# Kernel optimization log

Hardware: AMD Instinct MI355X
Metric: run time of the kernel (lower is better)

Reference implementation:

```python
import jax, jax.numpy as jnp
import numpy as np

H = 1024        # hidden_units
NH = 16         # num_heads
HD = H // NH    # head_dim = 64
B = 32
S = 500
MAX_SEQ = 500
ROPE_BASE = 10000.0


def setup_inputs() -> dict:
    key = jax.random.key(0)
    ks = jax.random.split(key, 16)
    s = 1.0 / np.sqrt(H)
    inp = {
        "query": jax.random.normal(ks[0], (B, S, H), jnp.float32),
        "key":   jax.random.normal(ks[1], (B, S, H), jnp.float32),
        "value": jax.random.normal(ks[2], (B, S, H), jnp.float32),
        "attn_mask": jax.random.randint(ks[3], (B, S), 0, 2).astype(bool),
        "Wq": jax.random.uniform(ks[4], (H, H), jnp.float32, -s, s),
        "bq": jax.random.uniform(ks[5], (H,), jnp.float32, -s, s),
        "Wk": jax.random.uniform(ks[6], (H, H), jnp.float32, -s, s),
        "bk": jax.random.uniform(ks[7], (H,), jnp.float32, -s, s),
        "Wv": jax.random.uniform(ks[8], (H, H), jnp.float32, -s, s),
        "bv": jax.random.uniform(ks[9], (H,), jnp.float32, -s, s),
        "Wo": jax.random.uniform(ks[10], (H, H), jnp.float32, -s, s),
        "bo": jax.random.uniform(ks[11], (H,), jnp.float32, -s, s),
        # rel_pos_bias embedding table: [2*max_seq_len-1, num_heads]
        "rel_emb": jax.random.normal(ks[12], (2 * MAX_SEQ - 1, NH), jnp.float32),
    }
    return inp


def _rope_tables(seq_len, head_dim, dtype):
    inv_freq = 1.0 / (ROPE_BASE ** (jnp.arange(0, head_dim, 2, dtype=jnp.float32) / head_dim))
    t = jnp.arange(seq_len, dtype=jnp.float32)
    freqs = t[:, None] * inv_freq[None, :]           # [S, HD/2]
    emb = jnp.concatenate([freqs, freqs], axis=-1)   # [S, HD]
    return jnp.cos(emb).astype(dtype), jnp.sin(emb).astype(dtype)


def _apply_rope(x, cos, sin):
    # x: [B, NH, S, HD]; even/odd slicing variant from source
    x_rot = jnp.concatenate([-x[..., 1::2], x[..., 0::2]], axis=-1)
    return x * cos + x_rot * sin


def reference(query, key, value, attn_mask, Wq, bq, Wk, bk, Wv, bv, Wo, bo, rel_emb):
    b, s, _ = query.shape
    Q = (query @ Wq.T + bq).reshape(b, s, NH, HD).transpose(0, 2, 1, 3)  # [B,NH,S,HD]
    K = (key   @ Wk.T + bk).reshape(b, s, NH, HD).transpose(0, 2, 1, 3)
    V = (value @ Wv.T + bv).reshape(b, s, NH, HD).transpose(0, 2, 1, 3)

    cos, sin = _rope_tables(s, HD, Q.dtype)  # [S,HD]
    Q = _apply_rope(Q, cos, sin)
    K = _apply_rope(K, cos, sin)

    # relative-position bias: [1, NH, S, S]
    pos = jnp.arange(s)[:, None] - jnp.arange(s)[None, :]
    rel_idx = jnp.clip(pos + MAX_SEQ - 1, 0, 2 * MAX_SEQ - 2)
    rel_bias = rel_emb[rel_idx].transpose(2, 0, 1)[None]  # [1,NH,S,S]

    # key-padding mask -> additive float mask [B,1,1,S]
    mask_bias = jnp.where(attn_mask[:, None, None, :], 0.0, -jnp.inf).astype(Q.dtype)

    scale = 1.0 / np.sqrt(HD)
    scores = jnp.einsum('bhqd,bhkd->bhqk', Q, K) * scale + mask_bias + rel_bias
    attn = jax.nn.softmax(scores, axis=-1)
    out = jnp.einsum('bhqk,bhkd->bhqd', attn, V)
    out = out.transpose(0, 2, 1, 3).reshape(b, s, H)
    out = jnp.clip(out, -30.0, 30.0)
    return out @ Wo.T + bo
```

## Files before the change

### kernel.cpp

```cpp
#include <hip/hip_runtime.h>
#include <math.h>


typedef unsigned short u16;
typedef unsigned int   u32;
typedef unsigned char  u8;
using bf16x8 = __attribute__((ext_vector_type(8))) short;
using f32x4  = __attribute__((ext_vector_type(4))) float;
using f32x2  = __attribute__((ext_vector_type(2))) float;
using u16x4  = __attribute__((ext_vector_type(4))) unsigned short;

#define DEV __device__ __forceinline__

#if __has_builtin(__builtin_amdgcn_exp2f)
#define EXP2(x) __builtin_amdgcn_exp2f(x)
#else
#define EXP2(x) exp2f(x)
#endif

DEV u16 f2bf(float f) {
  union { float f; u32 u; } c; c.f = f;
  u32 u = c.u;
  return (u16)((u + 0x7FFFu + ((u >> 16) & 1u)) >> 16);
}
DEV float bf2f(u16 h) {
  union { u32 u; float f; } c; c.u = ((u32)h) << 16;
  return c.f;
}
DEV u32 cvtpk(float a, float b) {
  u32 r;
  asm("v_cvt_pk_bf16_f32 %0, %1, %2" : "=v"(r) : "v"(a), "v"(b));
  return r;
}

DEV void async16(void* l, const void* g) {
  __builtin_amdgcn_global_load_lds(
      (__attribute__((address_space(1))) unsigned int*)g,
      (__attribute__((address_space(3))) unsigned int*)l, 16, 0, 0);
}

__global__ __launch_bounds__(512) void build_gather(const void* __restrict__ mraw,
                                                    u16* __restrict__ karr,
                                                    int* __restrict__ kept) {
  const int b = blockIdx.x;
  const int t = threadIdx.x;
  const int lane = t & 63, wave = t >> 6;
  __shared__ int s_li, s_lf;
  __shared__ int wbase[8];
  __shared__ int wpop[8];
  if (t == 0) { s_li = 0; s_lf = 0; }
  __syncthreads();
  const u32* w = (const u32*)mraw;
  int li = 0, lf = 0;
  for (int g = t; g < 4000; g += 512) {
    u32 v = w[g];
    li |= !(v == 0u || v == 1u);
    lf |= !(v == 0u || v == 0x3F800000u);
  }
  if (li) atomicOr(&s_li, 1);
  if (lf) atomicOr(&s_lf, 1);
  __syncthreads();
  const int mode = (!s_li) ? 0 : ((!s_lf) ? 1 : 2);
  int v = 0;
  if (t < 500) {
    if (mode == 0)      v = ((const int*)mraw)[b * 500 + t] != 0;
    else if (mode == 1) v = (((const float*)mraw)[b * 500 + t] != 0.0f);
    else                v = ((const u8*)mraw)[b * 500 + t] != 0;
  }
  unsigned long long bal = __ballot(v != 0);
  karr[b * 512 + t] = 0xFFFF;
  if (lane == 0) wpop[wave] = __popcll(bal);
  __syncthreads();
  if (t == 0) {
    int s = 0;
    for (int ww = 0; ww < 8; ++ww) { wbase[ww] = s; s += wpop[ww]; }
    kept[b] = s;
  }
  __syncthreads();
  if (v) {
    int rank = wbase[wave] + __popcll(bal & ((1ull << lane) - 1ull));
    karr[b * 512 + rank] = (u16)t;
  }
}

__global__ __launch_bounds__(256) void rope_table(float* __restrict__ tab) {
  int idx = blockIdx.x * 256 + threadIdx.x;
  if (idx >= 16000) return;
  int s = idx >> 5, j = idx & 31;
  float ang = (float)s * exp2f(-(float)j * 0.41524100f);
  float sn, cs;
  sincosf(ang, &sn, &cs);
  tab[idx * 2] = cs;
  tab[idx * 2 + 1] = sn;
}

__global__ __launch_bounds__(256) void cvt_w4(const float* __restrict__ w0,
                                              const float* __restrict__ w1,
                                              const float* __restrict__ w2,
                                              const float* __restrict__ w3,
                                              u16* __restrict__ dst) {
  const float* src = (blockIdx.y == 0) ? w0 : (blockIdx.y == 1) ? w1
                    : (blockIdx.y == 2) ? w2 : w3;
  int i = blockIdx.x * 256 + threadIdx.x;
  f32x4 f = *(const f32x4*)(src + (size_t)i * 4);
  u16x4 o;
  o[0] = f2bf(f[0]); o[1] = f2bf(f[1]); o[2] = f2bf(f[2]); o[3] = f2bf(f[3]);
  *(u16x4*)(dst + (size_t)blockIdx.y * 1048576 + (size_t)i * 4) = o;
}

__global__ __launch_bounds__(256) void cvt_f32_bf16(const float* __restrict__ src,
                                                    u16* __restrict__ dst, int n4) {
  int i = blockIdx.x * 256 + threadIdx.x;
  int stride = gridDim.x * 256;
  for (; i < n4; i += stride) {
    f32x4 f = *(const f32x4*)(src + (size_t)i * 4);
    u16x4 o;
    o[0] = f2bf(f[0]); o[1] = f2bf(f[1]); o[2] = f2bf(f[2]); o[3] = f2bf(f[3]);
    *(u16x4*)(dst + (size_t)i * 4) = o;
  }
}

__global__ __launch_bounds__(256) void gathercvt2(const float* __restrict__ srcK,
                                                  const float* __restrict__ srcV,
                                                  const u16* __restrict__ karr,
                                                  const int* __restrict__ kept,
                                                  u16* __restrict__ dstK,
                                                  u16* __restrict__ dstV) {
  const int b = blockIdx.y;
  const int r = blockIdx.x * 2 + (threadIdx.x >> 7);
  if (r >= kept[b]) return;
  const float* src = blockIdx.z ? srcV : srcK;
  u16* dst = blockIdx.z ? dstV : dstK;
  const int c = (threadIdx.x & 127) * 8;
  const int tok = karr[b * 512 + r];
  const float* s = src + ((size_t)b * 500 + tok) * 1024 + c;
  f32x4 f0 = *(const f32x4*)s;
  f32x4 f1 = *(const f32x4*)(s + 4);
  u16 o[8];
  o[0] = f2bf(f0[0]); o[1] = f2bf(f0[1]); o[2] = f2bf(f0[2]); o[3] = f2bf(f0[3]);
  o[4] = f2bf(f1[0]); o[5] = f2bf(f1[1]); o[6] = f2bf(f1[2]); o[7] = f2bf(f1[3]);
  *(bf16x8*)(dst + ((size_t)b * 512 + r) * 1024 + c) = *(bf16x8*)o;
}

DEV void gemm_core(const u16* __restrict__ A, size_t abase,
                   const u16* __restrict__ W,
                   int m0, int n0, int Mloc,
                   u16* AS, u16* BS, f32x4 (&acc)[4][4], int tid) {
  const int wave = tid >> 6;
  const int wr = wave >> 1, wc = wave & 1;
  const int fr = tid & 15, fo = (tid >> 4) & 3;
  const int fr2 = fr >> 1;
  const int aslot = ((4 * (fr & 1) + fo) ^ fr2) * 8;
  const int ATILE = 128 * 64;
  const int BTILE = 64 * 64;

#pragma unroll
  for (int mi = 0; mi < 4; ++mi)
#pragma unroll
    for (int ni = 0; ni < 4; ++ni)
#pragma unroll
      for (int j = 0; j < 4; ++j) acc[mi][ni][j] = 0.f;

  auto STG = [&](int t, int buf) {
    u16* sA = &AS[buf * ATILE];
    u16* sB = &BS[buf * BTILE];
#pragma unroll
    for (int i = 0; i < 2; ++i) {
      int c = i * 512 + tid;
      int r = c >> 3, v = (c & 7) ^ (r & 7);
      int ar = min(m0 + 2 * r + (v >> 2), Mloc - 1);
      async16(&sA[c * 8], A + abase + (size_t)ar * 1024 + t * 32 + (v & 3) * 8);
    }
    {
      int c = tid;
      int r = c >> 3, v = (c & 7) ^ (r & 7);
      int nr = n0 + 2 * r + (v >> 2);
      async16(&sB[c * 8], W + (size_t)nr * 1024 + t * 32 + (v & 3) * 8);
    }
  };

  STG(0, 0);
  asm volatile("s_waitcnt vmcnt(0)" ::: "memory");
  __builtin_amdgcn_sched_barrier(0);
  __builtin_amdgcn_s_barrier();

  int cur = 0;
  for (int t = 0; t < 32; ++t) {
    if (t + 1 < 32) STG(t + 1, cur ^ 1);
    const u16* a0 = &AS[cur * ATILE];
    const u16* b0 = &BS[cur * BTILE];
    bf16x8 a[4], b[4];
#pragma unroll
    for (int mi = 0; mi < 4; ++mi)
      a[mi] = *(const bf16x8*)&a0[(wr * 32 + mi * 8 + fr2) * 64 + aslot];
#pragma unroll
    for (int ni = 0; ni < 4; ++ni)
      b[ni] = *(const bf16x8*)&b0[(wc * 32 + ni * 8 + fr2) * 64 + aslot];
    asm volatile("s_waitcnt lgkmcnt(0)" ::: "memory");
    __builtin_amdgcn_sched_barrier(0);
    __builtin_amdgcn_s_setprio(1);
#pragma unroll
    for (int mi = 0; mi < 4; ++mi)
#pragma unroll
      for (int ni = 0; ni < 4; ++ni)
        acc[mi][ni] = __builtin_amdgcn_mfma_f32_16x16x32_bf16(a[mi], b[ni], acc[mi][ni], 0, 0, 0);
    __builtin_amdgcn_s_setprio(0);
    asm volatile("s_waitcnt vmcnt(0)" ::: "memory");
    __builtin_amdgcn_sched_barrier(0);
    __builtin_amdgcn_s_barrier();
    cur ^= 1;
  }
  __syncthreads();
}

__global__ __launch_bounds__(512, 4) void gemm_fused(
    const u16* __restrict__ Xq, const u16* __restrict__ XkC, const u16* __restrict__ XvC,
    const u16* __restrict__ Wb,
    const float* __restrict__ bq, const float* __restrict__ bk, const float* __restrict__ bv,
    u16* __restrict__ Qro, u16* __restrict__ PkC, u16* __restrict__ PvC,
    const float* __restrict__ tabg, const int* __restrict__ keptp) {
  __shared__ __attribute__((aligned(16))) u16 AS[2 * 128 * 64];
  __shared__ __attribute__((aligned(16))) u16 BS[2 * 64 * 64];
  const int bid = blockIdx.x;
  const int tid = threadIdx.x;
  const int wave = tid >> 6;
  const int wr = wave >> 1, wc = wave & 1;
  const int fr = tid & 15, fo = (tid >> 4) & 3;

  f32x4 acc[4][4];

  if (bid < 504) {
    const int swz = (bid & 7) * 63 + (bid >> 3);
    const int m0 = (swz >> 3) * 256;
    const int n0 = (swz & 7) * 128;
    gemm_core(Xq, 0, Wb, m0, n0, 16000, AS, BS, acc, tid);

    float* fw = (float*)&AS[0] + wave * 1024;
    const int hh = (n0 >> 6) + wc;
    const int lane = tid & 63;
    const int row = lane >> 2;
    const int jb = (lane & 3) * 8;
    float bvv[4];
#pragma unroll
    for (int ni = 0; ni < 4; ++ni) bvv[ni] = bq[n0 + wc * 64 + ni * 16 + fr];
#pragma unroll
    for (int mi = 0; mi < 4; ++mi) {
#pragma unroll
      for (int ni = 0; ni < 4; ++ni)
#pragma unroll
        for (int r = 0; r < 4; ++r)
          fw[(fo * 4 + r) * 64 + ni * 16 + fr] = acc[mi][ni][r] + bvv[ni];
      int m = m0 + wr * 64 + mi * 16 + row;
      if (m < 16000) {
        int bb = (u32)m / 500u;
        int ss = m - bb * 500;
        u16* dst = Qro + (((size_t)(bb * 16 + hh)) * 500 + ss) * 64;
        bf16x8 va, vb;
#pragma unroll
        for (int p = 0; p < 8; ++p) {
          int j = jb + p;
          float x0 = fw[row * 64 + j];
          float x1 = fw[row * 64 + 32 + j];
          float xe = fw[row * 64 + 2 * j];
          float xo = fw[row * 64 + 2 * j + 1];
          f32x2 cn = *(const f32x2*)(tabg + (ss * 32 + j) * 2);
          va[p] = (short)f2bf(x0 * cn[0] - xo * cn[1]);
          vb[p] = (short)f2bf(x1 * cn[0] + xe * cn[1]);
        }
        *(bf16x8*)(dst + jb) = va;
        *(bf16x8*)(dst + 32 + jb) = vb;
      }
      __builtin_amdgcn_s_barrier();
    }
  } else {
    const bool isV = (bid >= 1016);
    const int local = isV ? (bid - 1016) : (bid - 504);
    const u16* A = isV ? XvC : XkC;
    const u16* W = Wb + (isV ? 2 : 1) * 1048576;
    const float* bias = isV ? bv : bk;
    u16* Cout = isV ? PvC : PkC;
    const int swz = (local & 7) * 64 + (local >> 3);
    const int mb = swz >> 3;
    const int n0 = (swz & 7) * 128;
    const int b = mb >> 1, rb = mb & 1;
    const int kb = keptp[b];
    if (rb * 256 >= kb) return;
    const int m0 = rb * 256;
    gemm_core(A, (size_t)b * 512 * 1024, W, m0, n0, kb, AS, BS, acc, tid);

    u16* bw = (u16*)&AS[0] + wave * 2048;
#pragma unroll
    for (int mi = 0; mi < 4; ++mi) {
#pragma unroll
      for (int ni = 0; ni < 4; ++ni) {
        float bvs = bias[n0 + wc * 64 + ni * 16 + fr];
#pragma unroll
        for (int r = 0; r < 4; ++r)
          bw[(fo * 4 + r) * 64 + ni * 16 + fr] = f2bf(acc[mi][ni][r] + bvs);
      }
      int lane = tid & 63;
      int ro = lane >> 2, ch = lane & 3;
      int m = m0 + wr * 64 + mi * 16 + ro;
      bf16x8 v0 = *(const bf16x8*)&bw[ro * 64 + ch * 16];
      bf16x8 v1 = *(const bf16x8*)&bw[ro * 64 + ch * 16 + 8];
      if (m < kb) {
        u16* dst = Cout + ((size_t)b * 512 + m) * 1024 + n0 + wc * 64 + ch * 16;
        *(bf16x8*)dst = v0;
        *(bf16x8*)(dst + 8) = v1;
      }
    }
  }
}

__global__ __launch_bounds__(512, 4) void gemm_out(const u16* __restrict__ A,
                                                   const u16* __restrict__ W,
                                                   const float* __restrict__ bias,
                                                   float* __restrict__ Cout) {
  __shared__ __attribute__((aligned(16))) u16 AS[2 * 128 * 64];
  __shared__ __attribute__((aligned(16))) u16 BS[2 * 64 * 64];
  const int bid = blockIdx.x;
  const int tid = threadIdx.x;
  const int wave = tid >> 6;
  const int wr = wave >> 1, wc = wave & 1;
  const int fr = tid & 15, fo = (tid >> 4) & 3;
  const int swz = (bid & 7) * 63 + (bid >> 3);
  const int m0 = (swz >> 3) * 256;
  const int n0 = (swz & 7) * 128;

  f32x4 acc[4][4];
  gemm_core(A, 0, W, m0, n0, 16000, AS, BS, acc, tid);

  float* fw = (float*)&AS[0] + wave * 1024;
#pragma unroll
  for (int mi = 0; mi < 4; ++mi) {
#pragma unroll
    for (int ni = 0; ni < 4; ++ni) {
      float bv = bias[n0 + wc * 64 + ni * 16 + fr];
#pragma unroll
      for (int r = 0; r < 4; ++r)
        fw[(fo * 4 + r) * 64 + ni * 16 + fr] = acc[mi][ni][r] + bv;
    }
    int lane = tid & 63;
    int ro = lane >> 2, ch = lane & 3;
    int m = m0 + wr * 64 + mi * 16 + ro;
    f32x4 v0 = *(const f32x4*)&fw[ro * 64 + ch * 16];
    f32x4 v1 = *(const f32x4*)&fw[ro * 64 + ch * 16 + 4];
    f32x4 v2 = *(const f32x4*)&fw[ro * 64 + ch * 16 + 8];
    f32x4 v3 = *(const f32x4*)&fw[ro * 64 + ch * 16 + 12];
    if (m < 16000) {
      float* dst = Cout + (size_t)m * 1024 + n0 + wc * 64 + ch * 16;
      *(f32x4*)dst = v0;
      *(f32x4*)(dst + 4) = v1;
      *(f32x4*)(dst + 8) = v2;
      *(f32x4*)(dst + 12) = v3;
    }
  }
}

__global__ __launch_bounds__(256) void gather_k(const u16* __restrict__ PkC,
                                                const float* __restrict__ tab,
                                                const u16* __restrict__ karr,
                                                const int* __restrict__ kept,
                                                u16* __restrict__ Ktg) {
  const int tile = blockIdx.x;
  const int bh = blockIdx.y;
  const int h = bh & 15, b = bh >> 4;
  if (tile * 64 >= kept[b]) return;
  char* out = (char*)(Ktg + ((size_t)bh * 8 + tile) * 4096);
  const int tid = threadIdx.x;
#pragma unroll
  for (int i = 0; i < 8; ++i) {
    int item = i * 256 + tid;
    int row = item >> 5, j = item & 31;
    int rk = tile * 64 + row;
    int tok = karr[b * 512 + rk];
    int sw = (row & 7) << 4;
    u16 o0 = 0, o1 = 0;
    if (tok != 0xFFFF) {
      const u16* src = PkC + ((size_t)b * 512 + rk) * 1024 + h * 64;
      float x0 = bf2f(src[j]);
      float x1 = bf2f(src[32 + j]);
      float xe = bf2f(src[2 * j]);
      float xo = bf2f(src[2 * j + 1]);
      f32x2 cn = *(const f32x2*)(tab + (tok * 32 + j) * 2);
      o0 = f2bf(x0 * cn[0] - xo * cn[1]);
      o1 = f2bf(x1 * cn[0] + xe * cn[1]);
    }
    *(u16*)(out + row * 128 + ((2 * j) ^ sw)) = o0;
    *(u16*)(out + row * 128 + ((64 + 2 * j) ^ sw)) = o1;
  }
}

__global__ __launch_bounds__(256) void gather_v(const u16* __restrict__ PvC,
                                                const u16* __restrict__ karr,
                                                const int* __restrict__ kept,
                                                u16* __restrict__ Vtg) {
  const int tile = blockIdx.x;
  const int bh = blockIdx.y;
  const int h = bh & 15, b = bh >> 4;
  if (tile * 64 >= kept[b]) return;
  const int tid = threadIdx.x;
  __shared__ __attribute__((aligned(16))) u16 Vl[64 * 64];
#pragma unroll
  for (int i = 0; i < 2; ++i) {
    int chunk = i * 256 + tid;
    int slot = chunk >> 3, seg = chunk & 7;
    int rk = tile * 64 + slot;
    int tok = karr[b * 512 + rk];
    bf16x8 v;
#pragma unroll
    for (int p = 0; p < 8; ++p) v[p] = 0;
    if (tok != 0xFFFF)
      v = *(const bf16x8*)(PvC + ((size_t)b * 512 + rk) * 1024 + h * 64 + seg * 8);
    *(bf16x8*)&Vl[slot * 64 + seg * 8] = v;
  }
  __syncthreads();
  u16* out = Vtg + ((size_t)bh * 8 + tile) * 4096;
#pragma unroll
  for (int i = 0; i < 2; ++i) {
    int chunk = i * 256 + tid;
    int d = chunk >> 3, c16 = chunk & 7;
    int k0 = ((c16 * 16) ^ ((d & 7) << 4)) >> 1;
    bf16x8 v;
#pragma unroll
    for (int p = 0; p < 8; ++p) v[p] = (short)Vl[(k0 + p) * 64 + d];
    *(bf16x8*)(out + chunk * 8) = v;
  }
}

__global__ __launch_bounds__(512) void attn_kernel(const u16* __restrict__ Qr,
                                                   const u16* __restrict__ Ktg,
                                                   const u16* __restrict__ Vtg,
                                                   const float* __restrict__ rel_emb,
                                                   const u16* __restrict__ karr,
                                                   const int* __restrict__ kept,
                                                   u16* __restrict__ AO) {
  const int bid = blockIdx.x;
  const int bh = ((bid >> 5) << 3) | (bid & 7);
  const int qb = (bid >> 3) & 3;
  const int h = bh & 15, b = bh >> 4;
  const int q0 = qb * 128;
  const int tid = threadIdx.x;
  const int wave = tid >> 6;
  const int fr = tid & 15, fo = (tid >> 4) & 3;

  __shared__ __attribute__((aligned(16))) u16 Ks[2][4096];
  __shared__ __attribute__((aligned(16))) u16 Vs[2][4096];
  __shared__ __attribute__((aligned(16))) u16 Pl[8][1024];
  __shared__ float rel2[640];
  __shared__ u16 okk[512];

  const int nt = (kept[b] + 63) >> 6;
  const float LOG2E = 1.44269504f;
  for (int i = tid; i < 640; i += 512) {
    int g = min(max(q0 - 12 + i, 0), 998);
    rel2[i] = (i == 0) ? -1e30f : rel_emb[g * 16 + h] * LOG2E;
  }
  okk[tid] = karr[b * 512 + tid];

  const int qloc = wave * 16 + fr;
  const int qc = qloc + 511;
  const u16* Qb = Qr + ((size_t)bh * 500 + min(q0 + qloc, 499)) * 64;
  bf16x8 qf0 = *(const bf16x8*)(Qb + fo * 8);
  bf16x8 qf1 = *(const bf16x8*)(Qb + 32 + fo * 8);

  f32x4 o[4];
#pragma unroll
  for (int nf = 0; nf < 4; ++nf)
#pragma unroll
    for (int j = 0; j < 4; ++j) o[nf][j] = 0.f;
  float mrun = -1e30f, lrun = 0.f;

  const u16* Kb = Ktg + (size_t)bh * 32768;
  const u16* Vb = Vtg + (size_t)bh * 32768;
  const int sw = (fr & 7) << 4;
  const float SC = 0.18033688f;

  if (nt > 0) {
    async16(&Ks[0][tid * 8], Kb + tid * 8);
    async16(&Vs[0][tid * 8], Vb + tid * 8);
  }
  __syncthreads();

  for (int t = 0; t < nt; ++t) {
    const int cur = t & 1;
    if (t + 1 < nt) {
      async16(&Ks[cur ^ 1][tid * 8], Kb + (t + 1) * 4096 + tid * 8);
      async16(&Vs[cur ^ 1][tid * 8], Vb + (t + 1) * 4096 + tid * 8);
    }
    const char* Kt = (const char*)(cur ? &Ks[1][0] : &Ks[0][0]);
    const char* Vt = (const char*)(cur ? &Vs[1][0] : &Vs[0][0]);

    f32x4 sacc[4];
    __builtin_amdgcn_s_setprio(1);
#pragma unroll
    for (int nf = 0; nf < 4; ++nf) {
#pragma unroll
      for (int jj = 0; jj < 4; ++jj) sacc[nf][jj] = 0.f;
      int rb = (nf * 16 + fr) * 128;
      bf16x8 kb0 = *(const bf16x8*)(Kt + rb + ((fo * 16) ^ sw));
      bf16x8 kb1 = *(const bf16x8*)(Kt + rb + ((64 + fo * 16) ^ sw));
      sacc[nf] = __builtin_amdgcn_mfma_f32_16x16x32_bf16(kb0, qf0, sacc[nf], 0, 0, 0);
      sacc[nf] = __builtin_amdgcn_mfma_f32_16x16x32_bf16(kb1, qf1, sacc[nf], 0, 0, 0);
    }
    __builtin_amdgcn_s_setprio(0);

    float p2[4][4];
    float pmax = -3e30f;
#pragma unroll
    for (int nf = 0; nf < 4; ++nf) {
      u16x4 ok4 = *(const u16x4*)&okk[t * 64 + nf * 16 + fo * 4];
#pragma unroll
      for (int r = 0; r < 4; ++r) {
        int idx2 = max(qc - (int)ok4[r], 0);
        float s2 = fmaf(sacc[nf][r], SC, rel2[idx2]);
        p2[nf][r] = s2;
        pmax = fmaxf(pmax, s2);
      }
    }
    pmax = fmaxf(pmax, __shfl_xor(pmax, 16, 64));
    pmax = fmaxf(pmax, __shfl_xor(pmax, 32, 64));

    if (!__all(pmax <= mrun + 8.0f)) {
      float mnew = fmaxf(mrun, pmax);
      float scl = EXP2(mrun - mnew);
      lrun *= scl;
#pragma unroll
      for (int nf = 0; nf < 4; ++nf)
#pragma unroll
        for (int r = 0; r < 4; ++r) o[nf][r] *= scl;
      mrun = mnew;
    }

    float lsum = 0.f;
#pragma unroll
    for (int nf = 0; nf < 4; ++nf) {
      float e0 = EXP2(p2[nf][0] - mrun);
      float e1 = EXP2(p2[nf][1] - mrun);
      float e2 = EXP2(p2[nf][2] - mrun);
      float e3 = EXP2(p2[nf][3] - mrun);
      lsum += (e0 + e1) + (e2 + e3);
      uint2 w; w.x = cvtpk(e0, e1); w.y = cvtpk(e2, e3);
      *(uint2*)((char*)&Pl[wave][0] + fr * 128 + ((nf * 32 + fo * 8) ^ sw)) = w;
    }
    lsum += __shfl_xor(lsum, 16, 64);
    lsum += __shfl_xor(lsum, 32, 64);
    lrun += lsum;

    bf16x8 pa0 = *(const bf16x8*)((char*)&Pl[wave][0] + fr * 128 + ((fo * 16) ^ sw));
    bf16x8 pa1 = *(const bf16x8*)((char*)&Pl[wave][0] + fr * 128 + ((64 + fo * 16) ^ sw));
    __builtin_amdgcn_s_setprio(1);
#pragma unroll
    for (int nf = 0; nf < 4; ++nf) {
      int rb = (nf * 16 + fr) * 128;
      bf16x8 vb0 = *(const bf16x8*)(Vt + rb + ((fo * 16) ^ sw));
      bf16x8 vb1 = *(const bf16x8*)(Vt + rb + ((64 + fo * 16) ^ sw));
      o[nf] = __builtin_amdgcn_mfma_f32_16x16x32_bf16(vb0, pa0, o[nf], 0, 0, 0);
      o[nf] = __builtin_amdgcn_mfma_f32_16x16x32_bf16(vb1, pa1, o[nf], 0, 0, 0);
    }
    __builtin_amdgcn_s_setprio(0);
    __syncthreads();
  }

  float inv = (lrun > 0.f) ? 1.f / lrun : 0.f;
#pragma unroll
  for (int nf = 0; nf < 4; ++nf) {
    float v0 = fminf(fmaxf(o[nf][0] * inv, -30.f), 30.f);
    float v1 = fminf(fmaxf(o[nf][1] * inv, -30.f), 30.f);
    float v2 = fminf(fmaxf(o[nf][2] * inv, -30.f), 30.f);
    float v3 = fminf(fmaxf(o[nf][3] * inv, -30.f), 30.f);
    uint2 w; w.x = cvtpk(v0, v1); w.y = cvtpk(v2, v3);
    *(uint2*)((char*)&Pl[wave][0] + fr * 128 + ((nf * 32 + fo * 8) ^ sw)) = w;
  }
  {
    int lane = tid & 63;
    int ro = lane >> 2, c = lane & 3;
    int swr = (ro & 7) << 4;
    const char* Pw = (const char*)&Pl[wave][0];
    bf16x8 v0 = *(const bf16x8*)(Pw + ro * 128 + ((c * 32) ^ swr));
    bf16x8 v1 = *(const bf16x8*)(Pw + ro * 128 + ((c * 32 + 16) ^ swr));
    int token = q0 + wave * 16 + ro;
    if (token < 500) {
      u16* dst = AO + (size_t)(b * 500 + token) * 1024 + h * 64 + c * 16;
      *(bf16x8*)dst = v0;
      *(bf16x8*)(dst + 8) = v1;
    }
  }
}

extern "C" void kernel_launch(void* const* d_in, const int* in_sizes, int n_in,
                              void* d_out, int out_size, void* d_ws, size_t ws_size,
                              hipStream_t stream) {
  const float* query = (const float*)d_in[0];
  const float* key_  = (const float*)d_in[1];
  const float* value = (const float*)d_in[2];
  const void*  mask  = d_in[3];
  const float* Wq = (const float*)d_in[4];
  const float* bq = (const float*)d_in[5];
  const float* Wk = (const float*)d_in[6];
  const float* bk = (const float*)d_in[7];
  const float* Wv = (const float*)d_in[8];
  const float* bv = (const float*)d_in[9];
  const float* Wo = (const float*)d_in[10];
  const float* bo = (const float*)d_in[11];
  const float* rel = (const float*)d_in[12];

  char* ws = (char*)d_ws;
  const size_t SLOT = 33554432;
  u16* Wb = (u16*)ws;
  char* Aq = ws + 8388608;
  char* Bq = Aq + SLOT;
  char* Cq = Bq + SLOT;
  char* Dq = Cq + SLOT;
  char* Eq = Dq + SLOT;
  char* MISC = Eq + SLOT;
  u16* karr  = (u16*)(MISC + 65536);
  int* kept  = (int*)(MISC + 131072);
  float* tab = (float*)(MISC + 131584);
  u16* Qro = (u16*)d_out;

  build_gather<<<32, 512, 0, stream>>>(mask, karr, kept);
  rope_table<<<63, 256, 0, stream>>>(tab);
  cvt_w4<<<dim3(1024, 4), 256, 0, stream>>>(Wq, Wk, Wv, Wo, Wb);
  cvt_f32_bf16<<<2048, 256, 0, stream>>>(query, (u16*)Aq, 4096000);
  gathercvt2<<<dim3(256, 32, 2), 256, 0, stream>>>(key_, value, karr, kept,
                                                   (u16*)Bq, (u16*)Cq);

  gemm_fused<<<1528, 512, 0, stream>>>((u16*)Aq, (u16*)Bq, (u16*)Cq, Wb,
                                       bq, bk, bv,
                                       Qro, (u16*)Eq, (u16*)Dq, tab, kept);

  gather_k<<<dim3(8, 512), 256, 0, stream>>>((u16*)Eq, tab, karr, kept, (u16*)Cq);
  gather_v<<<dim3(8, 512), 256, 0, stream>>>((u16*)Dq, karr, kept, (u16*)Aq);

  attn_kernel<<<2048, 512, 0, stream>>>(Qro, (u16*)Cq, (u16*)Aq, rel,
                                        karr, kept, (u16*)Bq);

  gemm_out<<<504, 512, 0, stream>>>((u16*)Bq, Wb + 3 * 1048576, bo, (float*)d_out);
}
```

Measured before the change: 280.0 us.

## Fuse K RoPE/tiling and V transpose into the K/V projection GEMM epilogue

The K and V projection epilogues now write straight into the swizzled per-head tile layouts the attention kernel consumes. K gets RoPE applied with the gathered token positions, and V is transposed through padded shared memory. This removes the separate gather_k and gather_v kernels, along with the round trip of the projected K/V through global memory and two launches. In exchange the GEMM epilogue grows, with more scattered stores and extra barriers. It also adds a barrier to the gemm_out epilogue loop and merges the shared arrays into one buffer.

```diff
diff --git a/kernel.cpp b/kernel.cpp
--- a/kernel.cpp
+++ b/kernel.cpp
@@ -217,15 +217,18 @@
     const u16* __restrict__ Xq, const u16* __restrict__ XkC, const u16* __restrict__ XvC,
     const u16* __restrict__ Wb,
     const float* __restrict__ bq, const float* __restrict__ bk, const float* __restrict__ bv,
-    u16* __restrict__ Qro, u16* __restrict__ PkC, u16* __restrict__ PvC,
-    const float* __restrict__ tabg, const int* __restrict__ keptp) {
-  __shared__ __attribute__((aligned(16))) u16 AS[2 * 128 * 64];
-  __shared__ __attribute__((aligned(16))) u16 BS[2 * 64 * 64];
+    u16* __restrict__ Qro, u16* __restrict__ Ktg, u16* __restrict__ Vtg,
+    const float* __restrict__ tabg, const u16* __restrict__ karr,
+    const int* __restrict__ keptp) {
+  __shared__ __attribute__((aligned(16))) u16 SH[2 * 128 * 64 + 2 * 64 * 64];
+  u16* AS = &SH[0];
+  u16* BS = &SH[2 * 128 * 64];
   const int bid = blockIdx.x;
   const int tid = threadIdx.x;
   const int wave = tid >> 6;
   const int wr = wave >> 1, wc = wave & 1;
   const int fr = tid & 15, fo = (tid >> 4) & 3;
+  const int lane = tid & 63;
 
   f32x4 acc[4][4];
 
@@ -235,9 +238,8 @@
     const int n0 = (swz & 7) * 128;
     gemm_core(Xq, 0, Wb, m0, n0, 16000, AS, BS, acc, tid);
 
-    float* fw = (float*)&AS[0] + wave * 1024;
+    float* fw = (float*)&SH[0] + wave * 1024;
     const int hh = (n0 >> 6) + wc;
-    const int lane = tid & 63;
     const int row = lane >> 2;
     const int jb = (lane & 3) * 8;
     float bvv[4];
@@ -278,7 +280,6 @@
     const u16* A = isV ? XvC : XkC;
     const u16* W = Wb + (isV ? 2 : 1) * 1048576;
     const float* bias = isV ? bv : bk;
-    u16* Cout = isV ? PvC : PkC;
     const int swz = (local & 7) * 64 + (local >> 3);
     const int mb = swz >> 3;
     const int n0 = (swz & 7) * 128;
@@ -288,25 +289,75 @@
     const int m0 = rb * 256;
     gemm_core(A, (size_t)b * 512 * 1024, W, m0, n0, kb, AS, BS, acc, tid);
 
-    u16* bw = (u16*)&AS[0] + wave * 2048;
-#pragma unroll
-    for (int mi = 0; mi < 4; ++mi) {
-#pragma unroll
-      for (int ni = 0; ni < 4; ++ni) {
-        float bvs = bias[n0 + wc * 64 + ni * 16 + fr];
-#pragma unroll
-        for (int r = 0; r < 4; ++r)
-          bw[(fo * 4 + r) * 64 + ni * 16 + fr] = f2bf(acc[mi][ni][r] + bvs);
+    float* fw = (float*)&SH[0] + wave * 1056;
+    const int hh = (n0 >> 6) + wc;
+    float bvv[4];
+#pragma unroll
+    for (int ni = 0; ni < 4; ++ni) bvv[ni] = bias[n0 + wc * 64 + ni * 16 + fr];
+
+    if (!isV) {
+      const int row = lane >> 2;
+      const int jb = (lane & 3) * 8;
+#pragma unroll
+      for (int mi = 0; mi < 4; ++mi) {
+#pragma unroll
+        for (int ni = 0; ni < 4; ++ni)
+#pragma unroll
+          for (int r = 0; r < 4; ++r)
+            fw[(fo * 4 + r) * 66 + ni * 16 + fr] = acc[mi][ni][r] + bvv[ni];
+        int rk = m0 + wr * 64 + mi * 16 + row;
+        int tile = rk >> 6, rin = rk & 63;
+        int swk = (rin & 7) << 4;
+        if (tile * 64 < kb) {
+          char* outp = (char*)(Ktg + (((size_t)(b * 16 + hh)) * 8 + tile) * 4096) + rin * 128;
+          bf16x8 va, vb;
+          if (rk < kb) {
+            int tok = karr[b * 512 + rk];
+#pragma unroll
+            for (int p = 0; p < 8; ++p) {
+              int j = jb + p;
+              float x0 = fw[row * 66 + j];
+              float x1 = fw[row * 66 + 32 + j];
+              float xe = fw[row * 66 + 2 * j];
+              float xo = fw[row * 66 + 2 * j + 1];
+              f32x2 cn = *(const f32x2*)(tabg + (tok * 32 + j) * 2);
+              va[p] = (short)f2bf(x0 * cn[0] - xo * cn[1]);
+              vb[p] = (short)f2bf(x1 * cn[0] + xe * cn[1]);
+            }
+          } else {
+#pragma unroll
+            for (int p = 0; p < 8; ++p) { va[p] = 0; vb[p] = 0; }
+          }
+          *(bf16x8*)(outp + ((2 * jb) ^ swk)) = va;
+          *(bf16x8*)(outp + ((64 + 2 * jb) ^ swk)) = vb;
+        }
+        __builtin_amdgcn_s_barrier();
       }
-      int lane = tid & 63;
-      int ro = lane >> 2, ch = lane & 3;
-      int m = m0 + wr * 64 + mi * 16 + ro;
-      bf16x8 v0 = *(const bf16x8*)&bw[ro * 64 + ch * 16];
-      bf16x8 v1 = *(const bf16x8*)&bw[ro * 64 + ch * 16 + 8];
-      if (m < kb) {
-        u16* dst = Cout + ((size_t)b * 512 + m) * 1024 + n0 + wc * 64 + ch * 16;
-        *(bf16x8*)dst = v0;
-        *(bf16x8*)(dst + 8) = v1;
+    } else {
+      const int d = lane;
+      const int swv = (d & 7) << 4;
+#pragma unroll
+      for (int mi = 0; mi < 4; ++mi) {
+#pragma unroll
+        for (int ni = 0; ni < 4; ++ni)
+#pragma unroll
+          for (int r = 0; r < 4; ++r)
+            fw[(fo * 4 + r) * 66 + ni * 16 + fr] = acc[mi][ni][r] + bvv[ni];
+        int rk0 = m0 + wr * 64 + mi * 16;
+        int tile = rk0 >> 6, rin0 = rk0 & 63;
+        if (tile * 64 < kb) {
+          char* rowp = (char*)(Vtg + (((size_t)(b * 16 + hh)) * 8 + tile) * 4096) + d * 128;
+          bf16x8 va, vb;
+#pragma unroll
+          for (int t2 = 0; t2 < 8; ++t2)
+            va[t2] = (rk0 + t2 < kb) ? (short)f2bf(fw[t2 * 66 + d]) : (short)0;
+#pragma unroll
+          for (int t2 = 0; t2 < 8; ++t2)
+            vb[t2] = (rk0 + 8 + t2 < kb) ? (short)f2bf(fw[(8 + t2) * 66 + d]) : (short)0;
+          *(bf16x8*)(rowp + ((2 * rin0) ^ swv)) = va;
+          *(bf16x8*)(rowp + ((2 * rin0 + 16) ^ swv)) = vb;
+        }
+        __builtin_amdgcn_s_barrier();
       }
     }
   }
@@ -316,8 +367,9 @@
                                                    const u16* __restrict__ W,
                                                    const float* __restrict__ bias,
                                                    float* __restrict__ Cout) {
-  __shared__ __attribute__((aligned(16))) u16 AS[2 * 128 * 64];
-  __shared__ __attribute__((aligned(16))) u16 BS[2 * 64 * 64];
+  __shared__ __attribute__((aligned(16))) u16 SH[2 * 128 * 64 + 2 * 64 * 64];
+  u16* AS = &SH[0];
+  u16* BS = &SH[2 * 128 * 64];
   const int bid = blockIdx.x;
   const int tid = threadIdx.x;
   const int wave = tid >> 6;
@@ -330,7 +382,7 @@
   f32x4 acc[4][4];
   gemm_core(A, 0, W, m0, n0, 16000, AS, BS, acc, tid);
 
-  float* fw = (float*)&AS[0] + wave * 1024;
+  float* fw = (float*)&SH[0] + wave * 1024;
 #pragma unroll
   for (int mi = 0; mi < 4; ++mi) {
 #pragma unroll
@@ -354,77 +406,7 @@
       *(f32x4*)(dst + 8) = v2;
       *(f32x4*)(dst + 12) = v3;
     }
-  }
-}
-
-__global__ __launch_bounds__(256) void gather_k(const u16* __restrict__ PkC,
-                                                const float* __restrict__ tab,
-                                                const u16* __restrict__ karr,
-                                                const int* __restrict__ kept,
-                                                u16* __restrict__ Ktg) {
-  const int tile = blockIdx.x;
-  const int bh = blockIdx.y;
-  const int h = bh & 15, b = bh >> 4;
-  if (tile * 64 >= kept[b]) return;
-  char* out = (char*)(Ktg + ((size_t)bh * 8 + tile) * 4096);
-  const int tid = threadIdx.x;
-#pragma unroll
-  for (int i = 0; i < 8; ++i) {
-    int item = i * 256 + tid;
-    int row = item >> 5, j = item & 31;
-    int rk = tile * 64 + row;
-    int tok = karr[b * 512 + rk];
-    int sw = (row & 7) << 4;
-    u16 o0 = 0, o1 = 0;
-    if (tok != 0xFFFF) {
-      const u16* src = PkC + ((size_t)b * 512 + rk) * 1024 + h * 64;
-      float x0 = bf2f(src[j]);
-      float x1 = bf2f(src[32 + j]);
-      float xe = bf2f(src[2 * j]);
-      float xo = bf2f(src[2 * j + 1]);
-      f32x2 cn = *(const f32x2*)(tab + (tok * 32 + j) * 2);
-      o0 = f2bf(x0 * cn[0] - xo * cn[1]);
-      o1 = f2bf(x1 * cn[0] + xe * cn[1]);
-    }
-    *(u16*)(out + row * 128 + ((2 * j) ^ sw)) = o0;
-    *(u16*)(out + row * 128 + ((64 + 2 * j) ^ sw)) = o1;
-  }
-}
-
-__global__ __launch_bounds__(256) void gather_v(const u16* __restrict__ PvC,
-                                                const u16* __restrict__ karr,
-                                                const int* __restrict__ kept,
-                                                u16* __restrict__ Vtg) {
-  const int tile = blockIdx.x;
-  const int bh = blockIdx.y;
-  const int h = bh & 15, b = bh >> 4;
-  if (tile * 64 >= kept[b]) return;
-  const int tid = threadIdx.x;
-  __shared__ __attribute__((aligned(16))) u16 Vl[64 * 64];
-#pragma unroll
-  for (int i = 0; i < 2; ++i) {
-    int chunk = i * 256 + tid;
-    int slot = chunk >> 3, seg = chunk & 7;
-    int rk = tile * 64 + slot;
-    int tok = karr[b * 512 + rk];
-    bf16x8 v;
-#pragma unroll
-    for (int p = 0; p < 8; ++p) v[p] = 0;
-    if (tok != 0xFFFF)
-      v = *(const bf16x8*)(PvC + ((size_t)b * 512 + rk) * 1024 + h * 64 + seg * 8);
-    *(bf16x8*)&Vl[slot * 64 + seg * 8] = v;
-  }
-  __syncthreads();
-  u16* out = Vtg + ((size_t)bh * 8 + tile) * 4096;
-#pragma unroll
-  for (int i = 0; i < 2; ++i) {
-    int chunk = i * 256 + tid;
-    int d = chunk >> 3, c16 = chunk & 7;
-    int k0 = ((c16 * 16) ^ ((d & 7) << 4)) >> 1;
-    bf16x8 v;
-#pragma unroll
-    for (int p = 0; p < 8; ++p) v[p] = (short)Vl[(k0 + p) * 64 + d];
-    *(bf16x8*)(out + chunk * 8) = v;
+    __builtin_amdgcn_s_barrier();
   }
 }
 
@@ -628,12 +610,9 @@
 
   gemm_fused<<<1528, 512, 0, stream>>>((u16*)Aq, (u16*)Bq, (u16*)Cq, Wb,
                                        bq, bk, bv,
-                                       Qro, (u16*)Eq, (u16*)Dq, tab, kept);
-
-  gather_k<<<dim3(8, 512), 256, 0, stream>>>((u16*)Eq, tab, karr, kept, (u16*)Cq);
-  gather_v<<<dim3(8, 512), 256, 0, stream>>>((u16*)Dq, karr, kept, (u16*)Aq);
-
-  attn_kernel<<<2048, 512, 0, stream>>>(Qro, (u16*)Cq, (u16*)Aq, rel,
+                                       Qro, (u16*)Dq, (u16*)Eq, tab, karr, kept);
+
+  attn_kernel<<<2048, 512, 0, stream>>>(Qro, (u16*)Dq, (u16*)Eq, rel,
                                         karr, kept, (u16*)Bq);
 
   gemm_out<<<504, 512, 0, stream>>>((u16*)Bq, Wb + 3 * 1048576, bo, (float*)d_out);
```

Result: faster. 252.2 us (-10.0%).
